# Performance work log

Measured on AMD Instinct MI355X. Metric: run time of the kernel, lower is better.

Reference implementation:

```python
import jax, jax.numpy as jnp
import numpy as np

T, B, D = 2048, 16, 1024

def setup_inputs() -> dict:
    key = jax.random.key(0)
    k1, k2, k3, k4 = jax.random.split(key, 4)
    # xavier-uniform-ish scale for weights
    lim = float(np.sqrt(6.0 / (D + D)))
    return {
        "x": jax.random.normal(k1, (T, B, D), dtype=jnp.float32),
        "h0": jax.random.normal(k2, (B, D), dtype=jnp.float32),
        "W_x": jax.random.uniform(k3, (D, D), jnp.float32, -lim, lim),
        "W_h": jax.random.uniform(k4, (D, D), jnp.float32, -lim, lim) * 0.5,
        "b": jnp.zeros((D,), jnp.float32),
        "log_alpha": jnp.log(jnp.float32(0.5)),
    }

def reference(x, h0, W_x, W_h, b, log_alpha):
    alpha = jnp.exp(log_alpha)
    # Precompute input projection for all timesteps: [T,B,D]
    Wx_all = jnp.einsum('tbd,ed->tbe', x, W_x) + b

    def step(h_prev, wx_t):
        pre_act = h_prev @ W_h.T + wx_t          # [B,D]
        h_new = h_prev + alpha * jnp.tanh(pre_act)
        out = h_new * jax.nn.silu(h_new)
        return h_new, (h_new, out)

    _, (hs, outs) = jax.lax.scan(step, h0, Wx_all)
    h = jnp.concatenate([h0[None], hs], axis=0)  # [T+1,B,D]
    return outs, h
```

## Files before the change

kernel.cpp:

```cpp
#include <hip/hip_runtime.h>
#include <math.h>


#define T_STEPS 2048
#define BATCH 16
#define DIM 1024
#define NWG 128
#define E_PER_WG 8
#define HS_STRIDE 257
#define RED_STRIDE 516

__global__ __launch_bounds__(256) void gemm_wx_kernel(
    const float* __restrict__ X,
    const float* __restrict__ W,
    const float* __restrict__ bias,
    float* __restrict__ C)
{
    const int K = DIM, N = DIM;
    __shared__ float Xs[64][17];
    __shared__ float Ws[64][17];
    const int tid = threadIdx.x;
    const int m0 = blockIdx.x * 64;
    const int n0 = blockIdx.y * 64;
    const int ty = tid >> 4;
    const int tx = tid & 15;
    float acc[4][4] = {};

    for (int k0 = 0; k0 < K; k0 += 16) {
#pragma unroll
        for (int i = 0; i < 4; i++) {
            int idx = tid + i * 256;
            int r = idx >> 4;
            int c = idx & 15;
            Xs[r][c] = X[(size_t)(m0 + r) * K + (k0 + c)];
            Ws[r][c] = W[(size_t)(n0 + r) * K + (k0 + c)];
        }
        __syncthreads();
#pragma unroll
        for (int kk = 0; kk < 16; kk++) {
            float a[4], w[4];
#pragma unroll
            for (int i = 0; i < 4; i++) a[i] = Xs[ty * 4 + i][kk];
#pragma unroll
            for (int j = 0; j < 4; j++) w[j] = Ws[tx * 4 + j][kk];
#pragma unroll
            for (int i = 0; i < 4; i++)
#pragma unroll
                for (int j = 0; j < 4; j++)
                    acc[i][j] += a[i] * w[j];
        }
        __syncthreads();
    }
#pragma unroll
    for (int i = 0; i < 4; i++) {
        int m = m0 + ty * 4 + i;
#pragma unroll
        for (int j = 0; j < 4; j++) {
            int n = n0 + tx * 4 + j;
            C[(size_t)m * N + n] = acc[i][j] + bias[n];
        }
    }
}

__global__ __launch_bounds__(256) void copy_h0_kernel(
    const float* __restrict__ h0, float* __restrict__ h)
{
    int i = blockIdx.x * 256 + threadIdx.x;
    if (i < BATCH * DIM) h[i] = h0[i];
}

__global__ void barrier_init_kernel(unsigned int* bar)
{
    if (threadIdx.x < 512) bar[threadIdx.x] = 0u;
}

__global__ __launch_bounds__(256, 1) void rnn_scan_kernel(
    const float* __restrict__ Wh,
    const float* __restrict__ log_alpha,
    float* __restrict__ outs,
    float* __restrict__ h,
    unsigned int* __restrict__ bar)
{
    __shared__ float4 whs4[E_PER_WG * HS_STRIDE];
    __shared__ float4 hs4[BATCH * HS_STRIDE];
    __shared__ float red[8 * RED_STRIDE];

    const int tid = threadIdx.x;
    const int wg = blockIdx.x;
    const int e0 = wg * E_PER_WG;

    const float4* wh4 = (const float4*)Wh;
#pragma unroll
    for (int i = 0; i < 8; i++) {
        int idx = tid + i * 256;
        int r = idx >> 8, f = idx & 255;
        whs4[r * HS_STRIDE + f] = wh4[(size_t)(e0 + r) * 256 + f];
    }

    const float alpha = expf(log_alpha[0]);

    const int pos = tid & 7;
    const int eg = pos & 1;
    const int bg = pos >> 1;
    const int ks = tid >> 3;

    const int f_el = tid & 7;
    const int f_b  = tid >> 3;
    const int f_eg = f_el >> 2, f_i = f_el & 3;
    const int f_bg = f_b >> 2,  f_j = f_b & 3;
    const int f_pos = f_eg + 2 * f_bg;
    const int rbase_rd = f_pos * RED_STRIDE + f_i * 4 + f_j;
    const int f_e = e0 + f_el;

    const float* hsF = (const float*)hs4;
    unsigned int root_target = 0u;

    for (int t = 0; t < T_STEPS; t++) {
        const size_t oidx = (size_t)t * (BATCH * DIM) + (size_t)f_b * DIM + f_e;
        float wx = 0.f;
        if (tid < 128) wx = outs[oidx];

        const float4* hp4 = (const float4*)(h + (size_t)t * (BATCH * DIM));
#pragma unroll
        for (int i = 0; i < 16; i++) {
            int idx = tid + i * 256;
            int b = idx >> 8, f = idx & 255;
            hs4[b * HS_STRIDE + f] = hp4[idx];
        }
        __syncthreads();

        float hprev = 0.f;
        if (tid < 128) hprev = hsF[f_b * (HS_STRIDE * 4) + f_e];

        float p[4][4] = {};
#pragma unroll
        for (int m = 0; m < 8; m++) {
            const int f4 = ks + m * 32;
            float4 w[4], hv[4];
#pragma unroll
            for (int i = 0; i < 4; i++) w[i] = whs4[(eg * 4 + i) * HS_STRIDE + f4];
#pragma unroll
            for (int j = 0; j < 4; j++) hv[j] = hs4[(bg * 4 + j) * HS_STRIDE + f4];
#pragma unroll
            for (int i = 0; i < 4; i++)
#pragma unroll
                for (int j = 0; j < 4; j++)
                    p[i][j] += w[i].x * hv[j].x + w[i].y * hv[j].y
                             + w[i].z * hv[j].z + w[i].w * hv[j].w;
        }

        {
            float4* red4 = (float4*)red;
            const int rbase4 = pos * (RED_STRIDE / 4) + ks * 4;
#pragma unroll
            for (int i = 0; i < 4; i++)
                red4[rbase4 + i] = make_float4(p[i][0], p[i][1], p[i][2], p[i][3]);
        }
        __syncthreads();

        if (tid < 128) {
            float s = 0.f;
#pragma unroll
            for (int k2 = 0; k2 < 32; k2++) s += red[rbase_rd + k2 * 16];
            const float pre = s + wx;
            const float hnew = hprev + alpha * tanhf(pre);
            __hip_atomic_store(
                &h[(size_t)(t + 1) * (BATCH * DIM) + (size_t)f_b * DIM + f_e],
                hnew, __ATOMIC_RELAXED, __HIP_MEMORY_SCOPE_AGENT);
            const float sig = 1.f / (1.f + expf(-hnew));
            outs[oidx] = hnew * hnew * sig;
        }
        __syncthreads();

        if (t + 1 < T_STEPS) {
            if (tid == 0) {
                unsigned int old = __hip_atomic_fetch_add(
                    &bar[(wg & 7) * 32], 1u, __ATOMIC_RELAXED, __HIP_MEMORY_SCOPE_AGENT);
                if ((old & 15u) == 15u) {
                    __hip_atomic_fetch_add(
                        &bar[256], 1u, __ATOMIC_RELAXED, __HIP_MEMORY_SCOPE_AGENT);
                }
                root_target += 8u;
                while (__hip_atomic_load(&bar[256], __ATOMIC_RELAXED,
                                         __HIP_MEMORY_SCOPE_AGENT) < root_target)
                    __builtin_amdgcn_s_sleep(1);
            }
            __syncthreads();
        }
    }
}

extern "C" void kernel_launch(void* const* d_in, const int* in_sizes, int n_in,
                              void* d_out, int out_size, void* d_ws, size_t ws_size,
                              hipStream_t stream) {
    const float* x         = (const float*)d_in[0];
    const float* h0        = (const float*)d_in[1];
    const float* W_x       = (const float*)d_in[2];
    const float* W_h       = (const float*)d_in[3];
    const float* bias      = (const float*)d_in[4];
    const float* log_alpha = (const float*)d_in[5];

    float* outs = (float*)d_out;
    float* h    = (float*)d_out + (size_t)T_STEPS * BATCH * DIM;
    unsigned int* bar = (unsigned int*)d_ws;

    dim3 ggrid(32768 / 64, DIM / 64);
    gemm_wx_kernel<<<ggrid, 256, 0, stream>>>(x, W_x, bias, outs);

    copy_h0_kernel<<<(BATCH * DIM + 255) / 256, 256, 0, stream>>>(h0, h);
    barrier_init_kernel<<<1, 512, 0, stream>>>(bar);

    rnn_scan_kernel<<<NWG, 256, 0, stream>>>(W_h, log_alpha, outs, h, bar);
}
```

Before: 11.29 ms.

## Split batch into independent domains with per-wave flag sync instead of global barrier

The scan kernel now runs 256 workgroups arranged as 8 batch domains, each handling 2 batch rows. Each workgroup keeps 32 rows of W_h in shared memory. Each wave publishes a per-step flag, and waits only on the 128 flags of its own domain, which replaces the two-level global atomic barrier and removes cross-domain coupling. h is read directly from global memory (cache) instead of being staged in LDS, and the reduction uses wave shuffles instead of an LDS reduction with block syncs. This cuts the synchronisation latency on the critical path per timestep. The costs are more workgroups than before, reliance on all of them being co-resident, and relaxed-ordering memory visibility that depends on the explicit waitcnt.

```diff
diff --git a/kernel.cpp b/kernel.cpp
--- a/kernel.cpp
+++ b/kernel.cpp
@@ -5,10 +5,15 @@
 #define T_STEPS 2048
 #define BATCH 16
 #define DIM 1024
-#define NWG 128
-#define E_PER_WG 8
-#define HS_STRIDE 257
-#define RED_STRIDE 516
+#define NDOM 8
+#define WPD 32
+#define NWG (NDOM * WPD)
+#define COLS 32
+#define WSTRIDE 257
+
+__device__ __forceinline__ float dot4(float4 a, float4 b) {
+    return a.x * b.x + a.y * b.y + a.z * b.z + a.w * b.w;
+}
 
 __global__ __launch_bounds__(256) void gemm_wx_kernel(
     const float* __restrict__ X,
@@ -69,9 +74,9 @@
     if (i < BATCH * DIM) h[i] = h0[i];
 }
 
-__global__ void barrier_init_kernel(unsigned int* bar)
-{
-    if (threadIdx.x < 512) bar[threadIdx.x] = 0u;
+__global__ void flag_init_kernel(unsigned int* flags)
+{
+    flags[threadIdx.x] = 0u;
 }
 
 __global__ __launch_bounds__(256, 1) void rnn_scan_kernel(
@@ -79,90 +84,100 @@
     const float* __restrict__ log_alpha,
     float* __restrict__ outs,
     float* __restrict__ h,
-    unsigned int* __restrict__ bar)
-{
-    __shared__ float4 whs4[E_PER_WG * HS_STRIDE];
-    __shared__ float4 hs4[BATCH * HS_STRIDE];
-    __shared__ float red[8 * RED_STRIDE];
+    unsigned int* __restrict__ flags)
+{
+    __shared__ float4 whs4[COLS * WSTRIDE];
 
     const int tid = threadIdx.x;
-    const int wg = blockIdx.x;
-    const int e0 = wg * E_PER_WG;
+    const int bid = blockIdx.x;
+    const int dom = bid & 7;
+    const int wgl = bid >> 3;
+    const int e0  = wgl * COLS;
+    const int b0  = dom * 2;
 
     const float4* wh4 = (const float4*)Wh;
 #pragma unroll
-    for (int i = 0; i < 8; i++) {
+    for (int i = 0; i < 32; i++) {
         int idx = tid + i * 256;
         int r = idx >> 8, f = idx & 255;
-        whs4[r * HS_STRIDE + f] = wh4[(size_t)(e0 + r) * 256 + f];
-    }
-
+        whs4[r * WSTRIDE + f] = wh4[(size_t)(e0 + r) * 256 + f];
+    }
     const float alpha = expf(log_alpha[0]);
-
-    const int pos = tid & 7;
-    const int eg = pos & 1;
-    const int bg = pos >> 1;
-    const int ks = tid >> 3;
-
-    const int f_el = tid & 7;
-    const int f_b  = tid >> 3;
-    const int f_eg = f_el >> 2, f_i = f_el & 3;
-    const int f_bg = f_b >> 2,  f_j = f_b & 3;
-    const int f_pos = f_eg + 2 * f_bg;
-    const int rbase_rd = f_pos * RED_STRIDE + f_i * 4 + f_j;
-    const int f_e = e0 + f_el;
-
-    const float* hsF = (const float*)hs4;
-    unsigned int root_target = 0u;
+    __syncthreads();
+
+    const int w    = tid >> 6;
+    const int lane = tid & 63;
+    const int kg   = lane >> 2;
+    const int pg   = lane & 3;
+
+    const int f_i  = lane >> 2;
+    const int f_pg = lane & 3;
+    const int f_b  = b0 + (f_i & 1);
+    const int f_e  = e0 + w * 8 + f_pg * 2 + (f_i >> 1);
+
+    const int wbase0 = (w * 8 + pg * 2 + 0) * WSTRIDE;
+    const int wbase1 = (w * 8 + pg * 2 + 1) * WSTRIDE;
+
+    unsigned int* const fl = flags + dom * 128;
+    const int own = wgl * 4 + w;
+    const bool skip0 = (lane == own);
+    const bool skip1 = (lane + 64 == own);
+    unsigned int* const ownp = fl + own;
+
+    unsigned int fv0 = __hip_atomic_load(&fl[lane],      __ATOMIC_RELAXED, __HIP_MEMORY_SCOPE_AGENT);
+    unsigned int fv1 = __hip_atomic_load(&fl[lane + 64], __ATOMIC_RELAXED, __HIP_MEMORY_SCOPE_AGENT);
 
     for (int t = 0; t < T_STEPS; t++) {
-        const size_t oidx = (size_t)t * (BATCH * DIM) + (size_t)f_b * DIM + f_e;
-        float wx = 0.f;
-        if (tid < 128) wx = outs[oidx];
-
-        const float4* hp4 = (const float4*)(h + (size_t)t * (BATCH * DIM));
-#pragma unroll
-        for (int i = 0; i < 16; i++) {
-            int idx = tid + i * 256;
-            int b = idx >> 8, f = idx & 255;
-            hs4[b * HS_STRIDE + f] = hp4[idx];
-        }
-        __syncthreads();
-
-        float hprev = 0.f;
-        if (tid < 128) hprev = hsF[f_b * (HS_STRIDE * 4) + f_e];
-
-        float p[4][4] = {};
-#pragma unroll
-        for (int m = 0; m < 8; m++) {
-            const int f4 = ks + m * 32;
-            float4 w[4], hv[4];
-#pragma unroll
-            for (int i = 0; i < 4; i++) w[i] = whs4[(eg * 4 + i) * HS_STRIDE + f4];
-#pragma unroll
-            for (int j = 0; j < 4; j++) hv[j] = hs4[(bg * 4 + j) * HS_STRIDE + f4];
-#pragma unroll
-            for (int i = 0; i < 4; i++)
-#pragma unroll
-                for (int j = 0; j < 4; j++)
-                    p[i][j] += w[i].x * hv[j].x + w[i].y * hv[j].y
-                             + w[i].z * hv[j].z + w[i].w * hv[j].w;
-        }
-
-        {
-            float4* red4 = (float4*)red;
-            const int rbase4 = pos * (RED_STRIDE / 4) + ks * 4;
-#pragma unroll
-            for (int i = 0; i < 4; i++)
-                red4[rbase4 + i] = make_float4(p[i][0], p[i][1], p[i][2], p[i][3]);
-        }
-        __syncthreads();
-
-        if (tid < 128) {
-            float s = 0.f;
-#pragma unroll
-            for (int k2 = 0; k2 < 32; k2++) s += red[rbase_rd + k2 * 16];
-            const float pre = s + wx;
+        for (;;) {
+            bool ok = (skip0 || fv0 >= (unsigned)t) && (skip1 || fv1 >= (unsigned)t);
+            if (__ballot(ok) == ~0ull) break;
+            __builtin_amdgcn_s_sleep(1);
+            fv0 = __hip_atomic_load(&fl[lane],      __ATOMIC_RELAXED, __HIP_MEMORY_SCOPE_AGENT);
+            fv1 = __hip_atomic_load(&fl[lane + 64], __ATOMIC_RELAXED, __HIP_MEMORY_SCOPE_AGENT);
+        }
+        __builtin_amdgcn_sched_barrier(0);
+
+        const float*  hp  = h + (size_t)t * (BATCH * DIM);
+        const float4* hp4 = (const float4*)hp;
+
+        float wx = 0.f, hprev = 0.f;
+        size_t oidx = 0;
+        if (lane < 16) {
+            oidx  = (size_t)t * (BATCH * DIM) + (size_t)f_b * DIM + f_e;
+            wx    = outs[oidx];
+            hprev = hp[(size_t)f_b * DIM + f_e];
+        }
+
+        float acc0 = 0.f, acc1 = 0.f, acc2 = 0.f, acc3 = 0.f;
+#pragma unroll
+        for (int sc = 0; sc < 4; sc++) {
+            const int k4b = sc * 64 + kg;
+#pragma unroll
+            for (int m = 0; m < 4; m++) {
+                const int k4 = k4b + 16 * m;
+                float4 hv0 = hp4[(b0 + 0) * 256 + k4];
+                float4 hv1 = hp4[(b0 + 1) * 256 + k4];
+                float4 w0  = whs4[wbase0 + k4];
+                float4 w1  = whs4[wbase1 + k4];
+                acc0 += dot4(w0, hv0);
+                acc1 += dot4(w0, hv1);
+                acc2 += dot4(w1, hv0);
+                acc3 += dot4(w1, hv1);
+            }
+        }
+
+#pragma unroll
+        for (int mask = 4; mask <= 32; mask <<= 1) {
+            acc0 += __shfl_xor(acc0, mask);
+            acc1 += __shfl_xor(acc1, mask);
+            acc2 += __shfl_xor(acc2, mask);
+            acc3 += __shfl_xor(acc3, mask);
+        }
+
+        if (lane < 16) {
+            float s = (f_i == 0) ? acc0 : (f_i == 1) ? acc1
+                    : (f_i == 2) ? acc2 : acc3;
+            const float pre  = s + wx;
             const float hnew = hprev + alpha * tanhf(pre);
             __hip_atomic_store(
                 &h[(size_t)(t + 1) * (BATCH * DIM) + (size_t)f_b * DIM + f_e],
@@ -170,23 +185,13 @@
             const float sig = 1.f / (1.f + expf(-hnew));
             outs[oidx] = hnew * hnew * sig;
         }
-        __syncthreads();
-
-        if (t + 1 < T_STEPS) {
-            if (tid == 0) {
-                unsigned int old = __hip_atomic_fetch_add(
-                    &bar[(wg & 7) * 32], 1u, __ATOMIC_RELAXED, __HIP_MEMORY_SCOPE_AGENT);
-                if ((old & 15u) == 15u) {
-                    __hip_atomic_fetch_add(
-                        &bar[256], 1u, __ATOMIC_RELAXED, __HIP_MEMORY_SCOPE_AGENT);
-                }
-                root_target += 8u;
-                while (__hip_atomic_load(&bar[256], __ATOMIC_RELAXED,
-                                         __HIP_MEMORY_SCOPE_AGENT) < root_target)
-                    __builtin_amdgcn_s_sleep(1);
-            }
-            __syncthreads();
-        }
+
+        fv0 = __hip_atomic_load(&fl[lane],      __ATOMIC_RELAXED, __HIP_MEMORY_SCOPE_AGENT);
+        fv1 = __hip_atomic_load(&fl[lane + 64], __ATOMIC_RELAXED, __HIP_MEMORY_SCOPE_AGENT);
+
+        asm volatile("s_waitcnt vmcnt(0)" ::: "memory");
+        __hip_atomic_store(ownp, (unsigned)(t + 1),
+                           __ATOMIC_RELAXED, __HIP_MEMORY_SCOPE_AGENT);
     }
 }
 
@@ -202,13 +207,13 @@
 
     float* outs = (float*)d_out;
     float* h    = (float*)d_out + (size_t)T_STEPS * BATCH * DIM;
-    unsigned int* bar = (unsigned int*)d_ws;
+    unsigned int* flags = (unsigned int*)d_ws;
 
     dim3 ggrid(32768 / 64, DIM / 64);
     gemm_wx_kernel<<<ggrid, 256, 0, stream>>>(x, W_x, bias, outs);
 
     copy_h0_kernel<<<(BATCH * DIM + 255) / 256, 256, 0, stream>>>(h0, h);
-    barrier_init_kernel<<<1, 512, 0, stream>>>(bar);
-
-    rnn_scan_kernel<<<NWG, 256, 0, stream>>>(W_h, log_alpha, outs, h, bar);
-}
+    flag_init_kernel<<<1, 1024, 0, stream>>>(flags);
+
+    rnn_scan_kernel<<<NWG, 256, 0, stream>>>(W_h, log_alpha, outs, h, flags);
+}
```

Measured after the change: 19.28 ms. 70.7% more time.
